# Performance work log

Measured on AMD Instinct MI355X. Metric: run time of the kernel, lower is better.

The kernel has to match this reference:

```python
import jax, jax.numpy as jnp
from jax import lax
import numpy as np


def setup_inputs() -> dict:
    key = jax.random.key(0)
    k1, k2 = jax.random.split(key)
    sat_features = jax.random.normal(k1, (128, 4, 64, 16), dtype=jnp.float32)  # [B_s, h, w, c]
    grd_features = jax.random.normal(k2, (128, 4, 64, 16), dtype=jnp.float32)  # [B_g, h, gw, c]
    return {"sat_features": sat_features, "grd_features": grd_features}


def reference(sat_features, grd_features):
    B_s, h, w, c = sat_features.shape
    B_g, gh, gw, gc = grd_features.shape
    assert h == gh and c == gc

    # --- corr: circular cross-correlation over width via conv2d ---
    n = gw - 1
    sat_pad = jnp.concatenate([sat_features, sat_features[:, :, :n, :]], axis=2)  # [B_s,h,w+n,c]
    rhs = jnp.transpose(grd_features, (1, 2, 3, 0))  # HWIO: [h,gw,c,B_g]
    out = lax.conv_general_dilated(
        sat_pad, rhs, window_strides=(1, 1), padding='VALID',
        dimension_numbers=('NHWC', 'HWIO', 'NHWC'))  # [B_s,1,w,B_g]
    corr = out[:, 0, :, :]                  # [B_s, w, B_g]
    orien = jnp.argmax(corr, axis=1)        # [B_s, B_g] int

    # --- crop_sat: circular-shift gather along width, crop to grd width ---
    shift = orien % w                                                   # [B_s,B_g]
    idx = (jnp.arange(gw)[None, None, :] + shift[:, :, None]) % w       # [B_s,B_g,gw]
    # gather: sat_crop[i,j,y,k,ch] = sat_features[i, y, idx[i,j,k], ch]
    sat_crop = jnp.take_along_axis(
        sat_features[:, None],              # [B_s,1,h,w,c]
        idx[:, :, None, :, None],           # [B_s,B_g,1,gw,1]
        axis=3)                             # -> [B_s,B_g,h,gw,c]

    # --- L2 normalize per (sat,grd) pair and squared-chord distance ---
    norm = jnp.sqrt(jnp.sum(sat_crop * sat_crop, axis=(2, 3, 4), keepdims=True))
    sat_matrix = sat_crop / jnp.maximum(norm, 1e-12)
    dot = jnp.sum(sat_matrix * grd_features[None], axis=(2, 3, 4))      # [B_s,B_g]
    distance = 2.0 - 2.0 * dot.T                                        # [B_g,B_s]

    return sat_features, grd_features, distance, orien
```

## Files before the change

kernel.cpp:

```cpp
#include <hip/hip_runtime.h>
#include <math.h>

typedef _Float16 f16;
typedef __attribute__((ext_vector_type(8))) _Float16 f16x8;
typedef __attribute__((ext_vector_type(16))) float f32x16;

#define DIST_OFF  1048576
#define ORI_OFF   1064960
#define SATP_STR  72
#define RSTR      66

#define MFMA(a,b,c) __builtin_amdgcn_mfma_f32_32x32x16_f16((a),(b),(c),0,0,0)

__global__ __launch_bounds__(256) void prep_k(const float* __restrict__ grd,
                                              f16* __restrict__ gHi, f16* __restrict__ gLo) {
    __shared__ f16 tH[8192], tL[8192];
    const int b = blockIdx.x;
    const int tid = threadIdx.x;
    const int g0 = (b & 7) * 16;
    const int kq = b >> 3;
    #pragma unroll
    for (int i = 0; i < 32; ++i) {
        int flat = i * 256 + tid;
        int g_l = flat >> 9;
        int r   = flat & 511;
        int h   = r >> 7;
        int j   = r & 127;
        float v = grd[(((g0 + g_l) * 4 + h) * 64 + kq * 8) * 16 + j];
        int k_l = (j >> 4) * 64 + h * 16 + (j & 15);
        f16 hv = (f16)v;
        int a = (k_l >> 3) * 128 + g_l * 8 + (k_l & 7);
        tH[a] = hv;
        tL[a] = (f16)(v - (float)hv);
    }
    __syncthreads();
    #pragma unroll
    for (int i = 0; i < 4; ++i) {
        int f = i * 256 + tid;
        int dst = (kq * 64 + (f >> 4)) * 128 + g0 + (f & 15);
        ((f16x8*)gHi)[dst] = *(const f16x8*)(tH + f * 8);
        ((f16x8*)gLo)[dst] = *(const f16x8*)(tL + f * 8);
    }
}

__global__ __launch_bounds__(1024, 4) void corr_k(const float* __restrict__ sat,
                                                  const f16* __restrict__ gHi,
                                                  const f16* __restrict__ gLo,
                                                  float* __restrict__ out,
                                                  const float4* __restrict__ satIn,
                                                  const float4* __restrict__ grdIn,
                                                  int fuse) {
    __shared__ __align__(16) unsigned char smem[67584];
    __shared__ float wred[16];
    __shared__ float rnormS;
    f16* sH = (f16*)smem;
    f16* sL = sH + 127 * SATP_STR;
    float* red = (float*)smem;

    const int tid = threadIdx.x;
    const int s  = blockIdx.x >> 1;
    const int gh = blockIdx.x & 1;
    const int wave = tid >> 6, lane = tid & 63;
    const int m = lane & 31, half = lane >> 5;
    const int jt = wave & 1, gt = (wave >> 1) & 1, kh = wave >> 2;

    if (fuse && tid < 512) {
        float4* o4 = (float4*)out;
        int i = blockIdx.x * 512 + tid;
        o4[i] = satIn[i];
        o4[131072 + i] = grdIn[i];
    }

    const float* satS = sat + s * 4096;
    float ssq = 0.f;
    #pragma unroll
    for (int r = 0; r < 4; ++r) {
        int idx = r * 1024 + tid;
        float v = satS[idx];
        int h = idx >> 10, w = (idx >> 4) & 63, c = idx & 15;
        int col = h * 16 + c;
        f16 hv = (f16)v, lv = (f16)(v - (float)hv);
        sH[w * SATP_STR + col] = hv;
        sL[w * SATP_STR + col] = lv;
        if (w < 63) { sH[(w + 64) * SATP_STR + col] = hv; sL[(w + 64) * SATP_STR + col] = lv; }
        ssq += v * v;
    }
    #pragma unroll
    for (int off = 32; off > 0; off >>= 1) ssq += __shfl_down(ssq, off, 64);
    if (lane == 0) wred[wave] = ssq;
    __syncthreads();
    if (tid == 0) {
        float t = 0.f;
        #pragma unroll
        for (int i = 0; i < 16; ++i) t += wred[i];
        rnormS = 1.f / fmaxf(sqrtf(t), 1e-12f);
    }

    const f16* Ah = sH + (jt * 32 + m) * SATP_STR + half * 8;
    const f16* Al = sL + (jt * 32 + m) * SATP_STR + half * 8;
    const f16x8* BH = (const f16x8*)gHi + half * 128 + gh * 64 + gt * 32 + m;
    const f16x8* BL = (const f16x8*)gLo + half * 128 + gh * 64 + gt * 32 + m;

    f32x16 accH, accX;
    #pragma unroll
    for (int r = 0; r < 16; ++r) { accH[r] = 0.f; accX[r] = 0.f; }

    const int t0 = kh * 64;
    #pragma unroll 4
    for (int t = t0; t < t0 + 64; ++t) {
        int ao = (t >> 2) * SATP_STR + (t & 3) * 16;
        f16x8 ah = *(const f16x8*)(Ah + ao);
        f16x8 al = *(const f16x8*)(Al + ao);
        f16x8 bh = BH[t * 256];
        f16x8 bl = BL[t * 256];
        accH = MFMA(ah, bh, accH);
        accX = MFMA(ah, bl, accX);
        accX = MFMA(al, bh, accX);
    }
    accH = accH + accX;

    __syncthreads();
    {
        float* row = red + kh * 4224 + (gt * 32 + m) * RSTR + jt * 32 + half * 4;
        #pragma unroll
        for (int q = 0; q < 4; ++q) {
            float2 u = { accH[4 * q],     accH[4 * q + 1] };
            float2 v = { accH[4 * q + 2], accH[4 * q + 3] };
            *(float2*)(row + q * 8)     = u;
            *(float2*)(row + q * 8 + 2) = v;
        }
    }
    __syncthreads();
    {
        int g = tid >> 4, q4 = (tid & 15) * 4;
        int base = g * RSTR + q4;
        float2 u = {0.f, 0.f}, v = {0.f, 0.f};
        #pragma unroll
        for (int k = 0; k < 4; ++k) {
            float2 a = *(const float2*)(red + k * 4224 + base);
            float2 b = *(const float2*)(red + k * 4224 + base + 2);
            u.x += a.x; u.y += a.y; v.x += b.x; v.y += b.y;
        }
        *(float2*)(red + base) = u;
        *(float2*)(red + base + 2) = v;
    }
    __syncthreads();

    if (tid < 64) {
        int g = tid;
        const float* row = red + g * RSTR;
        float best = row[0];
        int bj = 0;
        for (int j = 1; j < 64; ++j) {
            float v = row[j];
            if (v > best) { best = v; bj = j; }
        }
        float dot = best * rnormS;
        int gg = gh * 64 + g;
        out[DIST_OFF + gg * 128 + s] = 2.f - 2.f * dot;
        out[ORI_OFF + s * 128 + gg]  = (float)bj;
    }
}

__global__ void copy_k(const float4* __restrict__ a, const float4* __restrict__ b,
                       float4* __restrict__ out) {
    int i = blockIdx.x * 256 + threadIdx.x;
    out[i] = a[i];
    out[131072 + i] = b[i];
}

extern "C" void kernel_launch(void* const* d_in, const int* in_sizes, int n_in,
                              void* d_out, int out_size, void* d_ws, size_t ws_size,
                              hipStream_t stream) {
    const float* sat = (const float*)d_in[0];
    const float* grd = (const float*)d_in[1];
    float* out = (float*)d_out;

    const bool useWs = (ws_size >= (size_t)2 * 1024 * 1024);
    f16* gHi;
    f16* gLo;
    if (useWs) {
        gHi = (f16*)d_ws;
        gLo = gHi + 524288;
    } else {
        gHi = (f16*)out;
        gLo = (f16*)(out + 262144);
    }

    prep_k<<<64, 256, 0, stream>>>(grd, gHi, gLo);
    corr_k<<<256, 1024, 0, stream>>>(sat, gHi, gLo, out,
                                     (const float4*)sat, (const float4*)grd,
                                     useWs ? 1 : 0);
    if (!useWs)
        copy_k<<<512, 256, 0, stream>>>((const float4*)sat, (const float4*)grd, (float4*)out);
}
```

Baseline: 92.25 us.

## Split correlation across more smaller blocks and merge partial argmax in combine kernel

Correlation work is repartitioned from 256 blocks of 1024 threads into 1024 blocks of 512 threads, each covering a 32-wide shift half and a 32-grd quarter. Per-half argmax partials and the per-sat norms go to workspace, and a later kernel merges them and writes distance and orientation. The output copy moves out of corr_k into that merge kernel. This spreads the work over more CUs with a lighter per-block footprint, at the cost of redundant sat loads per block, an extra global round-trip for partials, and an additional launch in the fallback path.

```diff
diff --git a/kernel.cpp b/kernel.cpp
--- a/kernel.cpp
+++ b/kernel.cpp
@@ -7,6 +7,7 @@
 
 #define DIST_OFF  1048576
 #define ORI_OFF   1064960
+#define GRD_OFF   524288
 #define SATP_STR  72
 #define RSTR      66
 
@@ -43,39 +44,30 @@
     }
 }
 
-__global__ __launch_bounds__(1024, 4) void corr_k(const float* __restrict__ sat,
-                                                  const f16* __restrict__ gHi,
-                                                  const f16* __restrict__ gLo,
-                                                  float* __restrict__ out,
-                                                  const float4* __restrict__ satIn,
-                                                  const float4* __restrict__ grdIn,
-                                                  int fuse) {
-    __shared__ __align__(16) unsigned char smem[67584];
-    __shared__ float wred[16];
-    __shared__ float rnormS;
+__global__ __launch_bounds__(512, 8) void corr_k(const float* __restrict__ sat,
+                                                 const f16* __restrict__ gHi,
+                                                 const f16* __restrict__ gLo,
+                                                 float2* __restrict__ part,
+                                                 float* __restrict__ norms) {
+    __shared__ __align__(16) unsigned char smem[36864];
+    __shared__ float wred[8];
     f16* sH = (f16*)smem;
     f16* sL = sH + 127 * SATP_STR;
     float* red = (float*)smem;
 
     const int tid = threadIdx.x;
-    const int s  = blockIdx.x >> 1;
-    const int gh = blockIdx.x & 1;
-    const int wave = tid >> 6, lane = tid & 63;
+    const int bi = blockIdx.x;
+    const int s  = bi >> 3;
+    const int gq = (bi >> 1) & 3;
+    const int jh = bi & 1;
+    const int kh = tid >> 6, lane = tid & 63;
     const int m = lane & 31, half = lane >> 5;
-    const int jt = wave & 1, gt = (wave >> 1) & 1, kh = wave >> 2;
-
-    if (fuse && tid < 512) {
-        float4* o4 = (float4*)out;
-        int i = blockIdx.x * 512 + tid;
-        o4[i] = satIn[i];
-        o4[131072 + i] = grdIn[i];
-    }
 
     const float* satS = sat + s * 4096;
     float ssq = 0.f;
     #pragma unroll
-    for (int r = 0; r < 4; ++r) {
-        int idx = r * 1024 + tid;
+    for (int r = 0; r < 8; ++r) {
+        int idx = r * 512 + tid;
         float v = satS[idx];
         int h = idx >> 10, w = (idx >> 4) & 63, c = idx & 15;
         int col = h * 16 + c;
@@ -87,27 +79,28 @@
     }
     #pragma unroll
     for (int off = 32; off > 0; off >>= 1) ssq += __shfl_down(ssq, off, 64);
-    if (lane == 0) wred[wave] = ssq;
-    __syncthreads();
-    if (tid == 0) {
+    if (lane == 0) wred[kh] = ssq;
+    __syncthreads();
+    if (tid == 0 && gq == 0 && jh == 0) {
         float t = 0.f;
         #pragma unroll
-        for (int i = 0; i < 16; ++i) t += wred[i];
-        rnormS = 1.f / fmaxf(sqrtf(t), 1e-12f);
-    }
-
-    const f16* Ah = sH + (jt * 32 + m) * SATP_STR + half * 8;
-    const f16* Al = sL + (jt * 32 + m) * SATP_STR + half * 8;
-    const f16x8* BH = (const f16x8*)gHi + half * 128 + gh * 64 + gt * 32 + m;
-    const f16x8* BL = (const f16x8*)gLo + half * 128 + gh * 64 + gt * 32 + m;
+        for (int i = 0; i < 8; ++i) t += wred[i];
+        norms[s] = sqrtf(t);
+    }
+
+    const f16* Ah = sH + (jh * 32 + m) * SATP_STR + half * 8;
+    const f16* Al = Ah + 127 * SATP_STR;
+    const f16x8* BH = (const f16x8*)gHi + half * 128 + gq * 32 + m;
+    const f16x8* BL = (const f16x8*)gLo + half * 128 + gq * 32 + m;
 
     f32x16 accH, accX;
     #pragma unroll
     for (int r = 0; r < 16; ++r) { accH[r] = 0.f; accX[r] = 0.f; }
 
-    const int t0 = kh * 64;
-    #pragma unroll 4
-    for (int t = t0; t < t0 + 64; ++t) {
+    const int t0 = kh * 32;
+    #pragma unroll 8
+    for (int i = 0; i < 32; ++i) {
+        int t = t0 + i;
         int ao = (t >> 2) * SATP_STR + (t & 3) * 16;
         f16x8 ah = *(const f16x8*)(Ah + ao);
         f16x8 al = *(const f16x8*)(Al + ao);
@@ -121,24 +114,36 @@
 
     __syncthreads();
     {
-        float* row = red + kh * 4224 + (gt * 32 + m) * RSTR + jt * 32 + half * 4;
+        float* row = red + ((kh & 3) * 2112) + m * RSTR + half * 4;
+        if (kh >= 4) {
+            #pragma unroll
+            for (int q = 0; q < 4; ++q) {
+                *(float2*)(row + q * 8)     = (float2){ accH[4*q],   accH[4*q+1] };
+                *(float2*)(row + q * 8 + 2) = (float2){ accH[4*q+2], accH[4*q+3] };
+            }
+        }
+    }
+    __syncthreads();
+    if (kh < 4) {
+        float* row = red + kh * 2112 + m * RSTR + half * 4;
         #pragma unroll
         for (int q = 0; q < 4; ++q) {
-            float2 u = { accH[4 * q],     accH[4 * q + 1] };
-            float2 v = { accH[4 * q + 2], accH[4 * q + 3] };
-            *(float2*)(row + q * 8)     = u;
-            *(float2*)(row + q * 8 + 2) = v;
+            float2 a = *(float2*)(row + q * 8), b = *(float2*)(row + q * 8 + 2);
+            a.x += accH[4*q];   a.y += accH[4*q+1];
+            b.x += accH[4*q+2]; b.y += accH[4*q+3];
+            *(float2*)(row + q * 8)     = a;
+            *(float2*)(row + q * 8 + 2) = b;
         }
     }
     __syncthreads();
     {
-        int g = tid >> 4, q4 = (tid & 15) * 4;
-        int base = g * RSTR + q4;
+        int g = tid >> 4, j0 = (tid & 15) * 4;
+        int base = g * RSTR + j0;
         float2 u = {0.f, 0.f}, v = {0.f, 0.f};
         #pragma unroll
         for (int k = 0; k < 4; ++k) {
-            float2 a = *(const float2*)(red + k * 4224 + base);
-            float2 b = *(const float2*)(red + k * 4224 + base + 2);
+            float2 a = *(const float2*)(red + k * 2112 + base);
+            float2 b = *(const float2*)(red + k * 2112 + base + 2);
             u.x += a.x; u.y += a.y; v.x += b.x; v.y += b.y;
         }
         *(float2*)(red + base) = u;
@@ -146,27 +151,59 @@
     }
     __syncthreads();
 
-    if (tid < 64) {
+    if (tid < 32) {
         int g = tid;
         const float* row = red + g * RSTR;
         float best = row[0];
         int bj = 0;
-        for (int j = 1; j < 64; ++j) {
+        for (int j = 1; j < 32; ++j) {
             float v = row[j];
             if (v > best) { best = v; bj = j; }
         }
-        float dot = best * rnormS;
-        int gg = gh * 64 + g;
-        out[DIST_OFF + gg * 128 + s] = 2.f - 2.f * dot;
-        out[ORI_OFF + s * 128 + gg]  = (float)bj;
+        part[(s * 2 + jh) * 128 + gq * 32 + g] = (float2){ best, (float)(jh * 32 + bj) };
     }
 }
 
 __global__ void copy_k(const float4* __restrict__ a, const float4* __restrict__ b,
-                       float4* __restrict__ out) {
+                       float4* __restrict__ out4,
+                       const float2* __restrict__ part, const float* __restrict__ norms,
+                       float* __restrict__ out) {
+    const int bi = blockIdx.x;
+    if (bi < 512) {
+        int i = bi * 256 + threadIdx.x;
+        out4[i] = a[i];
+        out4[131072 + i] = b[i];
+        return;
+    }
+    int i = (bi - 512) * 256 + threadIdx.x;
+    int s = i >> 7, g = i & 127;
+    float2 p0 = part[(s * 2 + 0) * 128 + g];
+    float2 p1 = part[(s * 2 + 1) * 128 + g];
+    float best = p0.x, bj = p0.y;
+    if (p1.x > p0.x) { best = p1.x; bj = p1.y; }
+    float rn = 1.f / fmaxf(norms[s], 1e-12f);
+    out[DIST_OFF + g * 128 + s] = 2.f - 2.f * best * rn;
+    out[ORI_OFF + s * 128 + g]  = bj;
+}
+
+__global__ void combine_k(const float2* __restrict__ part, const float* __restrict__ norms,
+                          float* __restrict__ out) {
     int i = blockIdx.x * 256 + threadIdx.x;
-    out[i] = a[i];
-    out[131072 + i] = b[i];
+    int s = i >> 7, g = i & 127;
+    float2 p0 = part[(s * 2 + 0) * 128 + g];
+    float2 p1 = part[(s * 2 + 1) * 128 + g];
+    float best = p0.x, bj = p0.y;
+    if (p1.x > p0.x) { best = p1.x; bj = p1.y; }
+    float rn = 1.f / fmaxf(norms[s], 1e-12f);
+    out[DIST_OFF + g * 128 + s] = 2.f - 2.f * best * rn;
+    out[ORI_OFF + s * 128 + g]  = bj;
+}
+
+__global__ void copy_only_k(const float4* __restrict__ a, const float4* __restrict__ b,
+                            float4* __restrict__ out4) {
+    int i = blockIdx.x * 256 + threadIdx.x;
+    out4[i] = a[i];
+    out4[131072 + i] = b[i];
 }
 
 extern "C" void kernel_launch(void* const* d_in, const int* in_sizes, int n_in,
@@ -176,21 +213,28 @@
     const float* grd = (const float*)d_in[1];
     float* out = (float*)d_out;
 
-    const bool useWs = (ws_size >= (size_t)2 * 1024 * 1024);
-    f16* gHi;
-    f16* gLo;
+    const bool useWs = (ws_size >= (size_t)(2 * 1024 * 1024 + 140 * 1024));
+    f16* gHi; f16* gLo; float2* part; float* norms;
     if (useWs) {
-        gHi = (f16*)d_ws;
-        gLo = gHi + 524288;
+        gHi   = (f16*)d_ws;
+        gLo   = gHi + 524288;
+        part  = (float2*)(gLo + 524288);
+        norms = (float*)(part + 32768);
     } else {
-        gHi = (f16*)out;
-        gLo = (f16*)(out + 262144);
+        gHi   = (f16*)out;
+        gLo   = (f16*)(out + 262144);
+        part  = (float2*)(out + GRD_OFF);
+        norms = (float*)(out + GRD_OFF + 65536);
     }
 
     prep_k<<<64, 256, 0, stream>>>(grd, gHi, gLo);
-    corr_k<<<256, 1024, 0, stream>>>(sat, gHi, gLo, out,
-                                     (const float4*)sat, (const float4*)grd,
-                                     useWs ? 1 : 0);
-    if (!useWs)
-        copy_k<<<512, 256, 0, stream>>>((const float4*)sat, (const float4*)grd, (float4*)out);
-}
+    corr_k<<<1024, 512, 0, stream>>>(sat, gHi, gLo, part, norms);
+    if (useWs) {
+        copy_k<<<576, 256, 0, stream>>>((const float4*)sat, (const float4*)grd,
+                                        (float4*)out, part, norms, out);
+    } else {
+        combine_k<<<64, 256, 0, stream>>>(part, norms, out);
+        copy_only_k<<<512, 256, 0, stream>>>((const float4*)sat, (const float4*)grd,
+                                             (float4*)out);
+    }
+}
```

Result: slower. 95.07 us (+3.1%).
